# Kernel tuning notes

Measured on AMD Instinct MI355X. Metric: run time of the kernel, lower is better.

## Reference

```python
import jax, jax.numpy as jnp
import numpy as np


def _rmsnorm(x):
    # F.rms_norm with no weight, default eps = finfo(dtype).eps
    eps = jnp.asarray(jnp.finfo(x.dtype).eps, x.dtype)
    return x * jax.lax.rsqrt(jnp.mean(x * x, axis=-1, keepdims=True) + eps)


def _rope(x, cos, sin):
    d = x.shape[-1] // 2
    x1, x2 = x[..., :d], x[..., d:]
    return jnp.concatenate([x1 * cos + x2 * sin, -x1 * sin + x2 * cos], axis=-1)


def setup_inputs() -> dict:
    key = jax.random.key(0)
    ks = jax.random.split(key, 9)
    B, T, C, H, D = 4, 2048, 1024, 8, 128
    x = jax.random.normal(ks[0], (B, T, C), jnp.float32)
    ve = jax.random.normal(ks[1], (B, T, C), jnp.float32)
    cos = jax.random.uniform(ks[2], (1, T, 1, D // 2), jnp.float32)
    sin = jax.random.uniform(ks[3], (1, T, 1, D // 2), jnp.float32)
    s = 0.02
    Wq = jax.random.normal(ks[4], (C, C), jnp.float32) * s
    Wk = jax.random.normal(ks[5], (C, C), jnp.float32) * s
    Wv = jax.random.normal(ks[6], (C, C), jnp.float32) * s
    Wproj = jax.random.normal(ks[7], (C, C), jnp.float32) * s
    Wgate = jax.random.normal(ks[8], (H, 32), jnp.float32) * s
    return {"x": x, "ve": ve, "cos": cos, "sin": sin,
            "Wq": Wq, "Wk": Wk, "Wv": Wv, "Wproj": Wproj, "Wgate": Wgate,
            "window_size": 1024}


def reference(x, ve, cos, sin, Wq, Wk, Wv, Wproj, Wgate, window_size):
    B, T, C = x.shape
    H = Wgate.shape[0]
    D = C // H
    gate_ch = Wgate.shape[1]  # 32

    q = (x @ Wq.T).reshape(B, T, H, D)
    k = (x @ Wk.T).reshape(B, T, H, D)
    v = (x @ Wv.T).reshape(B, T, H, D)

    # value-embedding sigmoid gate: gate in (0, 2)
    gate = 2.0 * jax.nn.sigmoid(x[..., :gate_ch] @ Wgate.T)  # [B,T,H]
    v = v + gate[..., None] * ve.reshape(B, T, H, D)

    q = _rmsnorm(_rope(q, cos, sin))
    k = _rmsnorm(_rope(k, cos, sin))

    scale = jnp.asarray(D, q.dtype) ** -0.5
    scores = jnp.einsum("bqhd,bkhd->bhqk", q, k) * scale  # [B,H,T,T]

    pos = jnp.arange(T)
    row, col = pos[:, None], pos[None, :]
    mask = (col <= row) & (col >= row - window_size + 1)  # sliding causal window
    scores = jnp.where(mask, scores, -jnp.inf)
    attn = jax.nn.softmax(scores, axis=-1)

    y = jnp.einsum("bhqk,bkhd->bqhd", attn, v).reshape(B, T, C)
    return y @ Wproj.T
```

## Files before the change

### kernel.cpp

```cpp
#include <hip/hip_runtime.h>
#include <cstdint>
#include <cstddef>

typedef __bf16 bf16;
typedef __bf16 bf16x8 __attribute__((ext_vector_type(8)));
typedef float  f32x4  __attribute__((ext_vector_type(4)));

#define AS1 __attribute__((address_space(1)))
#define AS3 __attribute__((address_space(3)))

#define B_ 4
#define T_ 2048
#define C_ 1024
#define H_ 8
#define D_ 128
#define WIN_ 1024
#define PS_ 72

__global__ void cvt_kernel(const float* __restrict__ src, bf16* __restrict__ dst, int n) {
  int i = (blockIdx.x * 256 + threadIdx.x) * 8;
  if (i >= n) return;
  float4 a = *(const float4*)(src + i);
  float4 b = *(const float4*)(src + i + 4);
  bf16x8 o;
  o[0] = (bf16)a.x; o[1] = (bf16)a.y; o[2] = (bf16)a.z; o[3] = (bf16)a.w;
  o[4] = (bf16)b.x; o[5] = (bf16)b.y; o[6] = (bf16)b.z; o[7] = (bf16)b.w;
  *(bf16x8*)(dst + i) = o;
}

__global__ void cvt_w4(const float* __restrict__ w0, const float* __restrict__ w1,
                       const float* __restrict__ w2, const float* __restrict__ w3,
                       bf16* __restrict__ dst) {
  const int z = blockIdx.y;
  const float* src = (z == 0) ? w0 : (z == 1) ? w1 : (z == 2) ? w2 : w3;
  int i = (blockIdx.x * 256 + threadIdx.x) * 8;
  float4 a = *(const float4*)(src + i);
  float4 b = *(const float4*)(src + i + 4);
  bf16x8 o;
  o[0] = (bf16)a.x; o[1] = (bf16)a.y; o[2] = (bf16)a.z; o[3] = (bf16)a.w;
  o[4] = (bf16)b.x; o[5] = (bf16)b.y; o[6] = (bf16)b.z; o[7] = (bf16)b.w;
  *(bf16x8*)(dst + (size_t)z * (C_ * C_) + i) = o;
}

__device__ __forceinline__ void gemm_tile_compute(
    const bf16* __restrict__ A, const bf16* __restrict__ W,
    bf16* As, bf16* Bs, int m0, int n0, f32x4 acc[4][4])
{
  const int tid  = threadIdx.x;
  const int w    = tid >> 6;
  const int l    = tid & 63;
  const int quad = l >> 4;
  const int arow = l & 15;
  const int lrow = tid >> 3;
  const int lcol = ((tid & 7) ^ (lrow & 7)) * 8;
  const int wm = w >> 1, wn = w & 1;
  const int sw = (arow & 7);

  for (int kt = 0; kt < C_; kt += 64) {
    __syncthreads();
#pragma unroll
    for (int i = 0; i < 4; i++) {
      const bf16* ga = A + (size_t)(m0 + i * 32 + lrow) * C_ + kt + lcol;
      __builtin_amdgcn_global_load_lds((AS1 unsigned int*)ga,
          (AS3 unsigned int*)(As + i * 2048 + w * 512), 16, 0, 0);
      const bf16* gb = W + (size_t)(n0 + i * 32 + lrow) * C_ + kt + lcol;
      __builtin_amdgcn_global_load_lds((AS1 unsigned int*)gb,
          (AS3 unsigned int*)(Bs + i * 2048 + w * 512), 16, 0, 0);
    }
    __syncthreads();

#pragma unroll
    for (int ks = 0; ks < 2; ks++) {
      const int ch = ((ks * 4 + quad) ^ sw) * 8;
      bf16x8 af[4], bfr[4];
#pragma unroll
      for (int mt = 0; mt < 4; mt++)
        af[mt] = *(const bf16x8*)(As + (wm * 64 + mt * 16 + arow) * 64 + ch);
#pragma unroll
      for (int nt = 0; nt < 4; nt++)
        bfr[nt] = *(const bf16x8*)(Bs + (wn * 64 + nt * 16 + arow) * 64 + ch);
#pragma unroll
      for (int mt = 0; mt < 4; mt++)
#pragma unroll
        for (int nt = 0; nt < 4; nt++)
          acc[mt][nt] = __builtin_amdgcn_mfma_f32_16x16x32_bf16(af[mt], bfr[nt], acc[mt][nt], 0, 0, 0);
    }
  }
}

__global__ __launch_bounds__(256) void gemm_qkv(
    const bf16* __restrict__ xb, const bf16* __restrict__ wb,
    bf16* __restrict__ qh, bf16* __restrict__ kh, bf16* __restrict__ vh)
{
  __shared__ bf16 As[128 * 64];
  __shared__ bf16 Bs[128 * 64];
  const int z = blockIdx.z;
  const bf16* W = wb + (size_t)z * (C_ * C_);
  bf16* out = (z == 0) ? qh : (z == 1) ? kh : vh;
  const int m0 = blockIdx.y * 128, n0 = blockIdx.x * 128;

  f32x4 acc[4][4];
#pragma unroll
  for (int i = 0; i < 4; i++)
#pragma unroll
    for (int j = 0; j < 4; j++) acc[i][j] = (f32x4){0.f, 0.f, 0.f, 0.f};

  gemm_tile_compute(xb, W, As, Bs, m0, n0, acc);

  const int tid = threadIdx.x, w = tid >> 6, l = tid & 63;
  const int quad = l >> 4, lc = l & 15, wm = w >> 1, wn = w & 1;
#pragma unroll
  for (int mt = 0; mt < 4; mt++) {
#pragma unroll
    for (int nt = 0; nt < 4; nt++) {
      const int col = n0 + wn * 64 + nt * 16 + lc;
      const int h = col >> 7, d = col & 127;
#pragma unroll
      for (int r = 0; r < 4; r++) {
        const int row = m0 + wm * 64 + mt * 16 + quad * 4 + r;
        const int b = row >> 11, t = row & 2047;
        out[(((size_t)(b * H_ + h)) * T_ + t) * D_ + d] = (bf16)acc[mt][nt][r];
      }
    }
  }
}

__global__ __launch_bounds__(256) void gemm_proj(
    const bf16* __restrict__ yb, const bf16* __restrict__ wproj, float* __restrict__ out)
{
  __shared__ bf16 As[128 * 64];
  __shared__ bf16 Bs[128 * 64];
  const int m0 = blockIdx.y * 128, n0 = blockIdx.x * 128;

  f32x4 acc[4][4];
#pragma unroll
  for (int i = 0; i < 4; i++)
#pragma unroll
    for (int j = 0; j < 4; j++) acc[i][j] = (f32x4){0.f, 0.f, 0.f, 0.f};

  gemm_tile_compute(yb, wproj, As, Bs, m0, n0, acc);

  const int tid = threadIdx.x, w = tid >> 6, l = tid & 63;
  const int quad = l >> 4, lc = l & 15, wm = w >> 1, wn = w & 1;
#pragma unroll
  for (int mt = 0; mt < 4; mt++) {
#pragma unroll
    for (int nt = 0; nt < 4; nt++) {
      const int col = n0 + wn * 64 + nt * 16 + lc;
#pragma unroll
      for (int r = 0; r < 4; r++) {
        const int row = m0 + wm * 64 + mt * 16 + quad * 4 + r;
        out[(size_t)row * C_ + col] = acc[mt][nt][r];
      }
    }
  }
}

__global__ __launch_bounds__(256) void rope_gate_t(
    bf16* __restrict__ qh, bf16* __restrict__ kh, const bf16* __restrict__ vh,
    const float* __restrict__ x, const float* __restrict__ ve,
    const float* __restrict__ cosb, const float* __restrict__ sinb,
    const float* __restrict__ wg, bf16* __restrict__ vt)
{
  __shared__ float Tile[64 * 129];
  __shared__ float Gs[64];
  const int bh = blockIdx.y;
  const int t0 = blockIdx.x * 64;
  const int b = bh >> 3, h = bh & 7;
  const int tid = threadIdx.x;
  const int r = tid >> 2, p = tid & 3;
  const int t = t0 + r;
  const float eps = 1.1920929e-07f;
  const float QSC = 0.08838834764831845f * 1.4426950408889634f;

  {
    const float* xr = x + ((size_t)(b * T_ + t)) * C_ + p * 8;
    const float* wgr = wg + h * 32 + p * 8;
    float gp = 0.f;
#pragma unroll
    for (int j = 0; j < 8; j++) gp += xr[j] * wgr[j];
    gp += __shfl_xor(gp, 1);
    gp += __shfl_xor(gp, 2);
    if (p == 0) Gs[r] = 2.0f / (1.0f + __expf(-gp));
  }

  const float4* cp = (const float4*)(cosb + (size_t)t * 64 + p * 16);
  const float4* sp = (const float4*)(sinb + (size_t)t * 64 + p * 16);
#pragma unroll
  for (int zz = 0; zz < 2; zz++) {
    bf16* rowp = (zz == 0 ? qh : kh) + ((size_t)bh * T_ + t) * D_ + p * 16;
    bf16x8 a0 = *(const bf16x8*)(rowp);
    bf16x8 a1 = *(const bf16x8*)(rowp + 8);
    bf16x8 b0 = *(const bf16x8*)(rowp + 64);
    bf16x8 b1 = *(const bf16x8*)(rowp + 72);
    float o1[16], o2[16];
    float ss = 0.f;
#pragma unroll
    for (int c = 0; c < 4; c++) {
      float4 cv = cp[c], sv = sp[c];
      float cf[4] = {cv.x, cv.y, cv.z, cv.w};
      float sf[4] = {sv.x, sv.y, sv.z, sv.w};
#pragma unroll
      for (int j = 0; j < 4; j++) {
        const int e = c * 4 + j;
        const float x1 = (float)(e < 8 ? a0[e] : a1[e - 8]);
        const float x2 = (float)(e < 8 ? b0[e] : b1[e - 8]);
        o1[e] = x1 * cf[j] + x2 * sf[j];
        o2[e] = x2 * cf[j] - x1 * sf[j];
        ss += o1[e] * o1[e] + o2[e] * o2[e];
      }
    }
    ss += __shfl_xor(ss, 1);
    ss += __shfl_xor(ss, 2);
    const float sc = rsqrtf(ss * (1.0f / 128.0f) + eps) * (zz == 0 ? QSC : 1.0f);
    bf16x8 w0, w1, w2, w3;
#pragma unroll
    for (int e = 0; e < 8; e++) {
      w0[e] = (bf16)(o1[e] * sc); w1[e] = (bf16)(o1[e + 8] * sc);
      w2[e] = (bf16)(o2[e] * sc); w3[e] = (bf16)(o2[e + 8] * sc);
    }
    *(bf16x8*)(rowp) = w0; *(bf16x8*)(rowp + 8) = w1;
    *(bf16x8*)(rowp + 64) = w2; *(bf16x8*)(rowp + 72) = w3;
  }

  __syncthreads();
  {
    const float g = Gs[r];
    const bf16* vr = vh + ((size_t)bh * T_ + t) * D_ + p * 32;
    const float* ver = ve + ((size_t)(b * T_ + t)) * C_ + h * D_ + p * 32;
    float* tr = Tile + r * 129 + p * 32;
#pragma unroll
    for (int c = 0; c < 4; c++) {
      bf16x8 vv = *(const bf16x8*)(vr + c * 8);
      float4 e0 = *(const float4*)(ver + c * 8);
      float4 e1 = *(const float4*)(ver + c * 8 + 4);
      tr[c * 8 + 0] = (float)vv[0] + g * e0.x;
      tr[c * 8 + 1] = (float)vv[1] + g * e0.y;
      tr[c * 8 + 2] = (float)vv[2] + g * e0.z;
      tr[c * 8 + 3] = (float)vv[3] + g * e0.w;
      tr[c * 8 + 4] = (float)vv[4] + g * e1.x;
      tr[c * 8 + 5] = (float)vv[5] + g * e1.y;
      tr[c * 8 + 6] = (float)vv[6] + g * e1.z;
      tr[c * 8 + 7] = (float)vv[7] + g * e1.w;
    }
  }
  __syncthreads();

  {
    const int d = tid >> 1, half = tid & 1;
    bf16* outp = vt + (((size_t)bh) * D_ + d) * T_ + t0 + half * 32;
#pragma unroll
    for (int c = 0; c < 4; c++) {
      bf16x8 o;
#pragma unroll
      for (int j = 0; j < 8; j++)
        o[j] = (bf16)Tile[(half * 32 + c * 8 + j) * 129 + d];
      *(bf16x8*)(outp + c * 8) = o;
    }
  }
}

__global__ __launch_bounds__(256) void attn_mfma(
    const bf16* __restrict__ qh, const bf16* __restrict__ kh,
    const bf16* __restrict__ vt, bf16* __restrict__ yb)
{
  __shared__ bf16 Ks[64 * 128];
  __shared__ bf16 VTs[128 * 64];
  __shared__ bf16 Ps[4 * 32 * PS_];
  const int bid = blockIdx.x;
  const int xcd = bid & 7, local = bid >> 3;
  const int bh = xcd * 4 + (local >> 4);
  const int q0 = (local & 15) * 128;
  const int tid = threadIdx.x;
  const int w = tid >> 6, l = tid & 63;
  const int quad = l >> 4, l15 = l & 15;
  const int sw = l15 & 7;
  const float FMAX = 16.5f;

  bf16x8 qf[2][4];
  const bf16* qbase = qh + ((size_t)bh * T_ + q0 + w * 32 + l15) * D_;
#pragma unroll
  for (int mt = 0; mt < 2; mt++)
#pragma unroll
    for (int dk = 0; dk < 4; dk++)
      qf[mt][dk] = *(const bf16x8*)(qbase + mt * 16 * D_ + dk * 32 + quad * 8);

  f32x4 O[2][8];
  f32x4 lst[2];
#pragma unroll
  for (int mt = 0; mt < 2; mt++) {
    lst[mt] = (f32x4){0.f, 0.f, 0.f, 0.f};
#pragma unroll
    for (int dn = 0; dn < 8; dn++) O[mt][dn] = (f32x4){0.f, 0.f, 0.f, 0.f};
  }

  const int kt_lo = (q0 >= WIN_) ? ((q0 - (WIN_ - 1)) >> 6) : 0;
  const int kt_hi = (q0 + 127) >> 6;
  const bf16* kg = kh + (size_t)bh * T_ * D_;
  const bf16* vg = vt + (size_t)bh * D_ * T_;
  bf16* Pw = Ps + w * 32 * PS_;

  const int krow_s = w * 4 + (l >> 4);
  const int kcol_s = (l15 ^ (krow_s & 7)) * 8;
  const int vrow_s = w * 8 + (l >> 3);
  const int vcol_s = (((l & 7) ^ (vrow_s & 7))) * 8;

  for (int kt = kt_lo; kt <= kt_hi; kt++) {
    const int k0 = kt * 64;
    __syncthreads();
#pragma unroll
    for (int s = 0; s < 4; s++) {
      const bf16* gk = kg + (size_t)(k0 + s * 16 + krow_s) * D_ + kcol_s;
      __builtin_amdgcn_global_load_lds((AS1 unsigned int*)gk,
          (AS3 unsigned int*)(Ks + s * 2048 + w * 512), 16, 0, 0);
      const bf16* gv = vg + (size_t)(s * 32 + vrow_s) * T_ + k0 + vcol_s;
      __builtin_amdgcn_global_load_lds((AS1 unsigned int*)gv,
          (AS3 unsigned int*)(VTs + s * 2048 + w * 512), 16, 0, 0);
    }
    __syncthreads();

    f32x4 sv[2][4];
#pragma unroll
    for (int mt = 0; mt < 2; mt++)
#pragma unroll
      for (int nf = 0; nf < 4; nf++) sv[mt][nf] = (f32x4){0.f, 0.f, 0.f, 0.f};
#pragma unroll
    for (int dk = 0; dk < 4; dk++) {
      const int ch = ((dk * 4 + quad) ^ sw) * 8;
      bf16x8 kf[4];
#pragma unroll
      for (int nf = 0; nf < 4; nf++)
        kf[nf] = *(const bf16x8*)(Ks + (nf * 16 + l15) * 128 + ch);
#pragma unroll
      for (int mt = 0; mt < 2; mt++)
#pragma unroll
        for (int nf = 0; nf < 4; nf++)
          sv[mt][nf] = __builtin_amdgcn_mfma_f32_16x16x32_bf16(qf[mt][dk], kf[nf], sv[mt][nf], 0, 0, 0);
    }

    if (!((k0 + 63 <= q0) && (k0 >= q0 + 128 - WIN_))) {
#pragma unroll
      for (int mt = 0; mt < 2; mt++)
#pragma unroll
        for (int nf = 0; nf < 4; nf++) {
          const int kcol = k0 + nf * 16 + l15;
#pragma unroll
          for (int r = 0; r < 4; r++) {
            const int qrow = q0 + w * 32 + mt * 16 + quad * 4 + r;
            const bool ok = (kcol <= qrow) && (kcol > qrow - WIN_);
            sv[mt][nf][r] = ok ? sv[mt][nf][r] : -3.0e38f;
          }
        }
    }

#pragma unroll
    for (int mt = 0; mt < 2; mt++) {
#pragma unroll
      for (int nf = 0; nf < 4; nf++)
#pragma unroll
        for (int r = 0; r < 4; r++) {
          const float p = __builtin_amdgcn_exp2f(sv[mt][nf][r] - FMAX);
          sv[mt][nf][r] = p;
          lst[mt][r] += p;
        }
#pragma unroll
      for (int nf = 0; nf < 4; nf++)
#pragma unroll
        for (int r = 0; r < 4; r++)
          Pw[(mt * 16 + quad * 4 + r) * PS_ + nf * 16 + l15] = (bf16)sv[mt][nf][r];
    }

    asm volatile("" ::: "memory");

#pragma unroll
    for (int ks = 0; ks < 2; ks++) {
      const int ch = ((ks * 4 + quad) ^ sw) * 8;
      bf16x8 af0 = *(const bf16x8*)(Pw + l15 * PS_ + ks * 32 + quad * 8);
      bf16x8 af1 = *(const bf16x8*)(Pw + (16 + l15) * PS_ + ks * 32 + quad * 8);
#pragma unroll
      for (int dn = 0; dn < 8; dn++) {
        bf16x8 bfv = *(const bf16x8*)(VTs + (dn * 16 + l15) * 64 + ch);
        O[0][dn] = __builtin_amdgcn_mfma_f32_16x16x32_bf16(af0, bfv, O[0][dn], 0, 0, 0);
        O[1][dn] = __builtin_amdgcn_mfma_f32_16x16x32_bf16(af1, bfv, O[1][dn], 0, 0, 0);
      }
    }
  }

#pragma unroll
  for (int mt = 0; mt < 2; mt++)
#pragma unroll
    for (int off = 1; off < 16; off <<= 1)
#pragma unroll
      for (int r = 0; r < 4; r++) lst[mt][r] += __shfl_xor(lst[mt][r], off);

  const int b = bh >> 3, h = bh & 7;
#pragma unroll
  for (int mt = 0; mt < 2; mt++) {
    f32x4 inv;
#pragma unroll
    for (int r = 0; r < 4; r++) inv[r] = 1.0f / lst[mt][r];
#pragma unroll
    for (int dn = 0; dn < 8; dn++)
#pragma unroll
      for (int r = 0; r < 4; r++) {
        const int t = q0 + w * 32 + mt * 16 + quad * 4 + r;
        yb[((size_t)(b * T_ + t)) * C_ + h * D_ + dn * 16 + l15] = (bf16)(O[mt][dn][r] * inv[r]);
      }
  }
}

extern "C" void kernel_launch(void* const* d_in, const int* in_sizes, int n_in,
                              void* d_out, int out_size, void* d_ws, size_t ws_size,
                              hipStream_t stream) {
  const float* x     = (const float*)d_in[0];
  const float* ve    = (const float*)d_in[1];
  const float* cosb  = (const float*)d_in[2];
  const float* sinb  = (const float*)d_in[3];
  const float* Wq    = (const float*)d_in[4];
  const float* Wk    = (const float*)d_in[5];
  const float* Wv    = (const float*)d_in[6];
  const float* Wproj = (const float*)d_in[7];
  const float* Wg    = (const float*)d_in[8];

  char* ws = (char*)d_ws;
  bf16* xb = (bf16*)ws;
  bf16* wb = (bf16*)(ws + 16777216);
  bf16* qh = (bf16*)(ws + 25165824);
  bf16* kh = (bf16*)(ws + 41943040);
  bf16* vh = (bf16*)(ws + 58720256);
  bf16* vt = xb;
  bf16* yb = vh;

  const int NX = B_ * T_ * C_;
  const int NW = C_ * C_;

  cvt_kernel<<<NX / 8 / 256, 256, 0, stream>>>(x, xb, NX);
  cvt_w4<<<dim3(NW / 8 / 256, 4), 256, 0, stream>>>(Wq, Wk, Wv, Wproj, wb);

  gemm_qkv<<<dim3(C_ / 128, (B_ * T_) / 128, 3), 256, 0, stream>>>(xb, wb, qh, kh, vh);
  rope_gate_t<<<dim3(T_ / 64, B_ * H_), 256, 0, stream>>>(qh, kh, vh, x, ve, cosb, sinb, Wg, vt);
  attn_mfma<<<512, 256, 0, stream>>>(qh, kh, vt, yb);
  gemm_proj<<<dim3(C_ / 128, (B_ * T_) / 128), 256, 0, stream>>>(yb, wb + 3 * NW, (float*)d_out);
}
```

Before: 299.2 us.

## Fuse RoPE and RMSNorm into QKV GEMM epilogue; merge conversion kernels

The QKV GEMM epilogue now stages each 128x128 output tile (one full head) in shared memory and applies RoPE plus RMSNorm to Q and K before writing them out with coalesced vector stores. The old rope_gate_t kernel's read-modify-write of q and k is removed, leaving only the V gating and transpose in a smaller kernel. The x and weight fp32-to-bf16 conversions are merged into one launch. The cost is a larger shared-memory tile and an extra barrier plus rotary math in the GEMM epilogue.

```diff
diff --git a/kernel.cpp b/kernel.cpp
--- a/kernel.cpp
+++ b/kernel.cpp
@@ -16,30 +16,28 @@
 #define D_ 128
 #define WIN_ 1024
 #define PS_ 72
-
-__global__ void cvt_kernel(const float* __restrict__ src, bf16* __restrict__ dst, int n) {
-  int i = (blockIdx.x * 256 + threadIdx.x) * 8;
-  if (i >= n) return;
+#define TS_ 136
+
+__global__ void cvt_all(const float* __restrict__ x,
+                        const float* __restrict__ w0, const float* __restrict__ w1,
+                        const float* __restrict__ w2, const float* __restrict__ w3,
+                        bf16* __restrict__ xb, bf16* __restrict__ wb) {
+  const int y = blockIdx.y;
+  const float* src;
+  bf16* dst;
+  if (y < 8) { src = x + (size_t)y * 1048576; dst = xb + (size_t)y * 1048576; }
+  else {
+    const int z = y - 8;
+    src = (z == 0) ? w0 : (z == 1) ? w1 : (z == 2) ? w2 : w3;
+    dst = wb + (size_t)z * 1048576;
+  }
+  const int i = (blockIdx.x * 256 + threadIdx.x) * 8;
   float4 a = *(const float4*)(src + i);
   float4 b = *(const float4*)(src + i + 4);
   bf16x8 o;
   o[0] = (bf16)a.x; o[1] = (bf16)a.y; o[2] = (bf16)a.z; o[3] = (bf16)a.w;
   o[4] = (bf16)b.x; o[5] = (bf16)b.y; o[6] = (bf16)b.z; o[7] = (bf16)b.w;
   *(bf16x8*)(dst + i) = o;
-}
-
-__global__ void cvt_w4(const float* __restrict__ w0, const float* __restrict__ w1,
-                       const float* __restrict__ w2, const float* __restrict__ w3,
-                       bf16* __restrict__ dst) {
-  const int z = blockIdx.y;
-  const float* src = (z == 0) ? w0 : (z == 1) ? w1 : (z == 2) ? w2 : w3;
-  int i = (blockIdx.x * 256 + threadIdx.x) * 8;
-  float4 a = *(const float4*)(src + i);
-  float4 b = *(const float4*)(src + i + 4);
-  bf16x8 o;
-  o[0] = (bf16)a.x; o[1] = (bf16)a.y; o[2] = (bf16)a.z; o[3] = (bf16)a.w;
-  o[4] = (bf16)b.x; o[5] = (bf16)b.y; o[6] = (bf16)b.z; o[7] = (bf16)b.w;
-  *(bf16x8*)(dst + (size_t)z * (C_ * C_) + i) = o;
 }
 
 __device__ __forceinline__ void gemm_tile_compute(
@@ -90,14 +88,18 @@
 
 __global__ __launch_bounds__(256) void gemm_qkv(
     const bf16* __restrict__ xb, const bf16* __restrict__ wb,
+    const float* __restrict__ cosb, const float* __restrict__ sinb,
     bf16* __restrict__ qh, bf16* __restrict__ kh, bf16* __restrict__ vh)
 {
-  __shared__ bf16 As[128 * 64];
-  __shared__ bf16 Bs[128 * 64];
+  __shared__ bf16 Tile[128 * TS_];
+  bf16* As = Tile;
+  bf16* Bs = Tile + 8192;
+
   const int z = blockIdx.z;
   const bf16* W = wb + (size_t)z * (C_ * C_);
-  bf16* out = (z == 0) ? qh : (z == 1) ? kh : vh;
   const int m0 = blockIdx.y * 128, n0 = blockIdx.x * 128;
+  const int h = blockIdx.x;
+  const int bb = m0 >> 11, tbase = m0 & 2047;
 
   f32x4 acc[4][4];
 #pragma unroll
@@ -108,19 +110,78 @@
   gemm_tile_compute(xb, W, As, Bs, m0, n0, acc);
 
   const int tid = threadIdx.x, w = tid >> 6, l = tid & 63;
-  const int quad = l >> 4, lc = l & 15, wm = w >> 1, wn = w & 1;
-#pragma unroll
-  for (int mt = 0; mt < 4; mt++) {
+  const int quad = l >> 4, l15 = l & 15, wm = w >> 1, wn = w & 1;
+
+  __syncthreads();
+#pragma unroll
+  for (int mt = 0; mt < 4; mt++)
 #pragma unroll
     for (int nt = 0; nt < 4; nt++) {
-      const int col = n0 + wn * 64 + nt * 16 + lc;
-      const int h = col >> 7, d = col & 127;
+      const int col = wn * 64 + nt * 16 + l15;
 #pragma unroll
       for (int r = 0; r < 4; r++) {
-        const int row = m0 + wm * 64 + mt * 16 + quad * 4 + r;
-        const int b = row >> 11, t = row & 2047;
-        out[(((size_t)(b * H_ + h)) * T_ + t) * D_ + d] = (bf16)acc[mt][nt][r];
-      }
+        const int rowl = wm * 64 + mt * 16 + quad * 4 + r;
+        Tile[rowl * TS_ + col] = (bf16)acc[mt][nt][r];
+      }
+    }
+  __syncthreads();
+
+  const int r = tid >> 1, p = tid & 1;
+  const int t = tbase + r;
+
+  if (z == 2) {
+    bf16* outp = vh + (((size_t)(bb * H_ + h)) * T_ + t) * D_ + p * 64;
+    const bf16* tr = Tile + r * TS_ + p * 64;
+#pragma unroll
+    for (int c = 0; c < 8; c++)
+      *(bf16x8*)(outp + c * 8) = *(const bf16x8*)(tr + c * 8);
+  } else {
+    const float QSC = 0.08838834764831845f * 1.4426950408889634f;
+    const float eps = 1.1920929e-07f;
+    const bf16* t1 = Tile + r * TS_ + p * 32;
+    bf16x8 av[4], bv[4];
+#pragma unroll
+    for (int g = 0; g < 4; g++) {
+      av[g] = *(const bf16x8*)(t1 + g * 8);
+      bv[g] = *(const bf16x8*)(t1 + 64 + g * 8);
+    }
+    float4 c4[8], s4[8];
+    const float4* cp = (const float4*)(cosb + (size_t)t * 64 + p * 32);
+    const float4* sp = (const float4*)(sinb + (size_t)t * 64 + p * 32);
+#pragma unroll
+    for (int c = 0; c < 8; c++) { c4[c] = cp[c]; s4[c] = sp[c]; }
+
+    float ss = 0.f;
+#pragma unroll
+    for (int g = 0; g < 4; g++)
+#pragma unroll
+      for (int j = 0; j < 8; j++) {
+        const int e = g * 8 + j;
+        const float cf = ((const float*)&c4[e >> 2])[e & 3];
+        const float sf = ((const float*)&s4[e >> 2])[e & 3];
+        const float x1 = (float)av[g][j], x2 = (float)bv[g][j];
+        const float o1 = x1 * cf + x2 * sf;
+        const float o2 = x2 * cf - x1 * sf;
+        ss += o1 * o1 + o2 * o2;
+      }
+    ss += __shfl_xor(ss, 1);
+    const float sc = rsqrtf(ss * (1.0f / 128.0f) + eps) * (z == 0 ? QSC : 1.0f);
+
+    bf16* outp = (z == 0 ? qh : kh) + (((size_t)(bb * H_ + h)) * T_ + t) * D_ + p * 32;
+#pragma unroll
+    for (int g = 0; g < 4; g++) {
+      bf16x8 o1v, o2v;
+#pragma unroll
+      for (int j = 0; j < 8; j++) {
+        const int e = g * 8 + j;
+        const float cf = ((const float*)&c4[e >> 2])[e & 3];
+        const float sf = ((const float*)&s4[e >> 2])[e & 3];
+        const float x1 = (float)av[g][j], x2 = (float)bv[g][j];
+        o1v[j] = (bf16)((x1 * cf + x2 * sf) * sc);
+        o2v[j] = (bf16)((x2 * cf - x1 * sf) * sc);
+      }
+      *(bf16x8*)(outp + g * 8) = o1v;
+      *(bf16x8*)(outp + 64 + g * 8) = o2v;
     }
   }
 }
@@ -156,11 +217,10 @@
   }
 }
 
-__global__ __launch_bounds__(256) void rope_gate_t(
-    bf16* __restrict__ qh, bf16* __restrict__ kh, const bf16* __restrict__ vh,
-    const float* __restrict__ x, const float* __restrict__ ve,
-    const float* __restrict__ cosb, const float* __restrict__ sinb,
-    const float* __restrict__ wg, bf16* __restrict__ vt)
+__global__ __launch_bounds__(256) void gate_t(
+    const bf16* __restrict__ vh, const float* __restrict__ x,
+    const float* __restrict__ ve, const float* __restrict__ wg,
+    bf16* __restrict__ vt)
 {
   __shared__ float Tile[64 * 129];
   __shared__ float Gs[64];
@@ -170,8 +230,6 @@
   const int tid = threadIdx.x;
   const int r = tid >> 2, p = tid & 3;
   const int t = t0 + r;
-  const float eps = 1.1920929e-07f;
-  const float QSC = 0.08838834764831845f * 1.4426950408889634f;
 
   {
     const float* xr = x + ((size_t)(b * T_ + t)) * C_ + p * 8;
@@ -183,47 +241,8 @@
     gp += __shfl_xor(gp, 2);
     if (p == 0) Gs[r] = 2.0f / (1.0f + __expf(-gp));
   }
-
-  const float4* cp = (const float4*)(cosb + (size_t)t * 64 + p * 16);
-  const float4* sp = (const float4*)(sinb + (size_t)t * 64 + p * 16);
-#pragma unroll
-  for (int zz = 0; zz < 2; zz++) {
-    bf16* rowp = (zz == 0 ? qh : kh) + ((size_t)bh * T_ + t) * D_ + p * 16;
-    bf16x8 a0 = *(const bf16x8*)(rowp);
-    bf16x8 a1 = *(const bf16x8*)(rowp + 8);
-    bf16x8 b0 = *(const bf16x8*)(rowp + 64);
-    bf16x8 b1 = *(const bf16x8*)(rowp + 72);
-    float o1[16], o2[16];
-    float ss = 0.f;
-#pragma unroll
-    for (int c = 0; c < 4; c++) {
-      float4 cv = cp[c], sv = sp[c];
-      float cf[4] = {cv.x, cv.y, cv.z, cv.w};
-      float sf[4] = {sv.x, sv.y, sv.z, sv.w};
-#pragma unroll
-      for (int j = 0; j < 4; j++) {
-        const int e = c * 4 + j;
-        const float x1 = (float)(e < 8 ? a0[e] : a1[e - 8]);
-        const float x2 = (float)(e < 8 ? b0[e] : b1[e - 8]);
-        o1[e] = x1 * cf[j] + x2 * sf[j];
-        o2[e] = x2 * cf[j] - x1 * sf[j];
-        ss += o1[e] * o1[e] + o2[e] * o2[e];
-      }
-    }
-    ss += __shfl_xor(ss, 1);
-    ss += __shfl_xor(ss, 2);
-    const float sc = rsqrtf(ss * (1.0f / 128.0f) + eps) * (zz == 0 ? QSC : 1.0f);
-    bf16x8 w0, w1, w2, w3;
-#pragma unroll
-    for (int e = 0; e < 8; e++) {
-      w0[e] = (bf16)(o1[e] * sc); w1[e] = (bf16)(o1[e + 8] * sc);
-      w2[e] = (bf16)(o2[e] * sc); w3[e] = (bf16)(o2[e + 8] * sc);
-    }
-    *(bf16x8*)(rowp) = w0; *(bf16x8*)(rowp + 8) = w1;
-    *(bf16x8*)(rowp + 64) = w2; *(bf16x8*)(rowp + 72) = w3;
-  }
-
   __syncthreads();
+
   {
     const float g = Gs[r];
     const bf16* vr = vh + ((size_t)bh * T_ + t) * D_ + p * 32;
@@ -431,14 +450,12 @@
   bf16* vt = xb;
   bf16* yb = vh;
 
-  const int NX = B_ * T_ * C_;
   const int NW = C_ * C_;
 
-  cvt_kernel<<<NX / 8 / 256, 256, 0, stream>>>(x, xb, NX);
-  cvt_w4<<<dim3(NW / 8 / 256, 4), 256, 0, stream>>>(Wq, Wk, Wv, Wproj, wb);
-
-  gemm_qkv<<<dim3(C_ / 128, (B_ * T_) / 128, 3), 256, 0, stream>>>(xb, wb, qh, kh, vh);
-  rope_gate_t<<<dim3(T_ / 64, B_ * H_), 256, 0, stream>>>(qh, kh, vh, x, ve, cosb, sinb, Wg, vt);
+  cvt_all<<<dim3(512, 12), 256, 0, stream>>>(x, Wq, Wk, Wv, Wproj, xb, wb);
+  gemm_qkv<<<dim3(C_ / 128, (B_ * T_) / 128, 3), 256, 0, stream>>>(
+      xb, wb, cosb, sinb, qh, kh, vh);
+  gate_t<<<dim3(T_ / 64, B_ * H_), 256, 0, stream>>>(vh, x, ve, Wg, vt);
   attn_mfma<<<512, 256, 0, stream>>>(qh, kh, vt, yb);
   gemm_proj<<<dim3(C_ / 128, (B_ * T_) / 128), 256, 0, stream>>>(yb, wb + 3 * NW, (float*)d_out);
 }
```

Result: no change. 301.6 us (+0.8%).
